# Kernel optimization log

Measured on AMD Instinct MI355X. Metric: run time of the kernel, lower is better.

The kernel has to match this reference:

```python
import jax, jax.numpy as jnp
import numpy as np

NEG_INF = -1e30
D_MODEL = 128


def setup_inputs() -> dict:
    key = jax.random.key(0)
    k1, k2, k3 = jax.random.split(key, 3)
    B, D, Lc, Lq = 64, D_MODEL, 1024, 256
    C = jax.random.normal(k1, (B, D, Lc), dtype=jnp.float32)
    Q = jax.random.normal(k2, (B, D, Lq), dtype=jnp.float32)
    cmask = jnp.ones((B, Lc), dtype=jnp.float32)
    qmask = jnp.ones((B, Lq), dtype=jnp.float32)
    lim = (1.0 / D) ** 0.5
    w = jax.random.uniform(k3, (3 * D,), dtype=jnp.float32, minval=-lim, maxval=lim)
    return {"C": C, "Q": Q, "cmask": cmask, "qmask": qmask, "w": w}


def reference(C, Q, cmask, qmask, w):
    # C: (B, D, Lc), Q: (B, D, Lq), w: (3D,)
    D = C.shape[1]
    Ct = jnp.swapaxes(C, 1, 2)  # (B, Lc, D)
    Qt = jnp.swapaxes(Q, 1, 2)  # (B, Lq, D)
    w1, w2, w3 = w[:D], w[D:2 * D], w[2 * D:]
    # Decomposed trilinear similarity: equivalent to cat([Ct,Qt,Ct*Qt]) @ w
    S = (jnp.einsum('bld,d->bl', Ct, w1)[:, :, None]
         + jnp.einsum('bmd,d->bm', Qt, w2)[:, None, :]
         + jnp.einsum('bld,bmd->blm', Ct * w3, Qt))  # (B, Lc, Lq)
    qm = qmask[:, None, :]  # (B, 1, Lq)
    cm = cmask[:, :, None]  # (B, Lc, 1)
    S1 = jax.nn.softmax(S + (1.0 - qm) * NEG_INF, axis=2)
    S2 = jax.nn.softmax(S + (1.0 - cm) * NEG_INF, axis=1)
    A = jnp.einsum('blm,bmd->bld', S1, Qt)  # (B, Lc, D)
    S12 = jnp.einsum('blm,bnm->bln', S1, S2)  # (B, Lc, Lc)
    Bv = jnp.einsum('bln,bnd->bld', S12, Ct)  # (B, Lc, D)
    out = jnp.concatenate([Ct, A, Ct * A, Ct * Bv], axis=2)  # (B, Lc, 4D)
    # dropout is identity in eval mode
    return jnp.swapaxes(out, 1, 2)  # (B, 4D, Lc)
```

## Files before the change

### kernel.cpp

```cpp
#include <hip/hip_runtime.h>

#define NB  64
#define ND  128
#define NLC 1024
#define NLQ 256
#define FNEG (-1e30f)

typedef __bf16 bf16x8 __attribute__((ext_vector_type(8)));
typedef float f32x4 __attribute__((ext_vector_type(4)));

__device__ __forceinline__ ushort f2bf(float x) {
  unsigned u = __float_as_uint(x);
  return (ushort)((u + 0x7fffu + ((u >> 16) & 1u)) >> 16);
}
__device__ __forceinline__ float bf2f(ushort u) {
  return __uint_as_float((unsigned)u << 16);
}
__device__ __forceinline__ bf16x8 ldfrag(const ushort* p) {
  return *reinterpret_cast<const bf16x8*>(p);
}
__device__ __forceinline__ uint4 pack8(float a0, float a1, float a2, float a3,
                                       float a4, float a5, float a6, float a7) {
  uint4 pk;
  pk.x = (unsigned)f2bf(a0) | ((unsigned)f2bf(a1) << 16);
  pk.y = (unsigned)f2bf(a2) | ((unsigned)f2bf(a3) << 16);
  pk.z = (unsigned)f2bf(a4) | ((unsigned)f2bf(a5) << 16);
  pk.w = (unsigned)f2bf(a6) | ((unsigned)f2bf(a7) << 16);
  return pk;
}

__global__ __launch_bounds__(256) void convert_kernel(
    const float* __restrict__ C, const float* __restrict__ Q,
    const float* __restrict__ w,
    ushort* __restrict__ Ctw3, ushort* __restrict__ Qt16,
    ushort* __restrict__ Cn16, ushort* __restrict__ Qn16,
    float* __restrict__ c1part, float* __restrict__ q2part) {
  __shared__ float tile[64][65];
  __shared__ float cred[64][4];
  int b = blockIdx.y;
  int tid = blockIdx.x;
  int t = threadIdx.x, c = t & 63, r0 = t >> 6;
  if (tid < 32) {
    int d0 = (tid >> 4) * 64, l0 = (tid & 15) * 64;
    const float* src = C + (size_t)b * ND * NLC;
    float part = 0.f;
#pragma unroll
    for (int p = 0; p < 16; ++p) {
      int r = r0 + p * 4;
      float v = src[(size_t)(d0 + r) * NLC + l0 + c];
      tile[c][r] = v * w[2 * ND + d0 + r];
      part += v * w[d0 + r];
    }
    cred[c][r0] = part;
    __syncthreads();
    ushort* dst = Ctw3 + (size_t)b * NLC * ND;
#pragma unroll
    for (int p = 0; p < 16; ++p) {
      int r = r0 + p * 4;
      dst[(size_t)(l0 + r) * ND + d0 + c] = f2bf(tile[r][c]);
    }
    if (t < 64)
      c1part[(size_t)(tid >> 4) * NB * NLC + b * NLC + l0 + t] =
          cred[t][0] + cred[t][1] + cred[t][2] + cred[t][3];
  } else if (tid < 40) {
    int q = tid - 32;
    int d0 = (q >> 2) * 64, m0 = (q & 3) * 64;
    const float* src = Q + (size_t)b * ND * NLQ;
    float part = 0.f;
#pragma unroll
    for (int p = 0; p < 16; ++p) {
      int r = r0 + p * 4;
      float v = src[(size_t)(d0 + r) * NLQ + m0 + c];
      tile[c][r] = v;
      part += v * w[ND + d0 + r];
    }
    cred[c][r0] = part;
    __syncthreads();
    ushort* dst = Qt16 + (size_t)b * NLQ * ND;
#pragma unroll
    for (int p = 0; p < 16; ++p) {
      int r = r0 + p * 4;
      dst[(size_t)(m0 + r) * ND + d0 + c] = f2bf(tile[r][c]);
    }
    if (t < 64)
      q2part[(size_t)(q >> 2) * NB * NLQ + b * NLQ + m0 + t] =
          cred[t][0] + cred[t][1] + cred[t][2] + cred[t][3];
  } else if (tid < 56) {
    size_t ofs = (size_t)(tid - 40) * 8192;
    const float* src = C + (size_t)b * ND * NLC + ofs;
    ushort* dst = Cn16 + (size_t)b * ND * NLC + ofs;
#pragma unroll
    for (int it = 0; it < 4; ++it) {
      int e = (it * 256 + t) * 8;
      float4 v0 = *(const float4*)(src + e), v1 = *(const float4*)(src + e + 4);
      *(uint4*)(dst + e) = pack8(v0.x, v0.y, v0.z, v0.w, v1.x, v1.y, v1.z, v1.w);
    }
  } else {
    size_t ofs = (size_t)(tid - 56) * 16384;
    const float* src = Q + (size_t)b * ND * NLQ + ofs;
    ushort* dst = Qn16 + (size_t)b * ND * NLQ + ofs;
#pragma unroll
    for (int it = 0; it < 8; ++it) {
      int e = (it * 256 + t) * 8;
      float4 v0 = *(const float4*)(src + e), v1 = *(const float4*)(src + e + 4);
      *(uint4*)(dst + e) = pack8(v0.x, v0.y, v0.z, v0.w, v1.x, v1.y, v1.z, v1.w);
    }
  }
}

__global__ __launch_bounds__(512) void score_stats(
    const ushort* __restrict__ Ctw3, const ushort* __restrict__ Qt16,
    const float* __restrict__ c1part, const float* __restrict__ q2part,
    const float* __restrict__ cmask, const float* __restrict__ qmask,
    ushort* __restrict__ e1g, ushort* __restrict__ e1t,
    float* __restrict__ rscale_g, float* __restrict__ psum_part,
    float* __restrict__ chunkmax_g) {
  __shared__ union {
    struct { __align__(16) ushort As[128 * 32]; __align__(16) ushort Bs[256 * 32]; } s;
    __align__(16) ushort bounce[128 * 264];
    __align__(16) ushort bounce2[256 * 136];
  } u;
  __shared__ float rowred[128][4];
  __shared__ float rowsum[128][4];
  __shared__ float colred[256][2];
  __shared__ float rmaxs[128];
  __shared__ float rcs[128];
  __shared__ float cnegs[128];
  __shared__ float qnegs[256];
  __shared__ float c1s[128];
  __shared__ float q2s[256];
  __shared__ float chunkmax_s;

  int b = blockIdx.y, chunk = blockIdx.x, l0 = chunk * 128;
  int t = threadIdx.x, lane = t & 63, wid = t >> 6;
  int wy = wid >> 2, wx = wid & 3, ln = lane & 15, qd = lane >> 4;

  if (t < 128) {
    int idx = b * NLC + l0 + t;
    c1s[t] = c1part[idx] + c1part[NB * NLC + idx];
    cnegs[t] = (1.f - cmask[idx]) * FNEG;
  } else if (t < 384) {
    int m = t - 128;
    int idx = b * NLQ + m;
    q2s[m] = q2part[idx] + q2part[NB * NLQ + idx];
    qnegs[m] = (1.f - qmask[idx]) * FNEG;
  }

  const ushort* Ab = Ctw3 + (size_t)b * NLC * ND;
  const ushort* Bb = Qt16 + (size_t)b * NLQ * ND;
  f32x4 acc[4][4];
#pragma unroll
  for (int i = 0; i < 4; ++i)
#pragma unroll
    for (int j = 0; j < 4; ++j) acc[i][j] = (f32x4){0.f, 0.f, 0.f, 0.f};

  for (int kk = 0; kk < ND; kk += 32) {
#pragma unroll
    for (int p = 0; p < 3; ++p) {
      int e4 = p * 512 + t;
      if (e4 < 512) {
        int r = e4 >> 2, cc = (e4 & 3) * 8;
        *(int4*)(u.s.As + r * 32 + cc) = *(const int4*)(Ab + (size_t)(l0 + r) * ND + kk + cc);
      } else {
        int e = e4 - 512;
        int r = e >> 2, cc = (e & 3) * 8;
        *(int4*)(u.s.Bs + r * 32 + cc) = *(const int4*)(Bb + (size_t)r * ND + kk + cc);
      }
    }
    __syncthreads();
    bf16x8 af[4], bfr[4];
#pragma unroll
    for (int i = 0; i < 4; ++i) {
      af[i]  = ldfrag(u.s.As + (wy * 64 + i * 16 + ln) * 32 + qd * 8);
      bfr[i] = ldfrag(u.s.Bs + (wx * 64 + i * 16 + ln) * 32 + qd * 8);
    }
#pragma unroll
    for (int i = 0; i < 4; ++i)
#pragma unroll
      for (int j = 0; j < 4; ++j)
        acc[i][j] = __builtin_amdgcn_mfma_f32_16x16x32_bf16(af[i], bfr[j], acc[i][j], 0, 0, 0);
    __syncthreads();
  }

  float qnj[4], q2j[4];
#pragma unroll
  for (int j = 0; j < 4; ++j) {
    int m = wx * 64 + j * 16 + ln;
    qnj[j] = qnegs[m];
    q2j[j] = q2s[m];
  }
#pragma unroll
  for (int i = 0; i < 4; ++i)
#pragma unroll
    for (int r = 0; r < 4; ++r) {
      int ll = wy * 64 + i * 16 + qd * 4 + r;
      float cv = c1s[ll];
#pragma unroll
      for (int j = 0; j < 4; ++j) acc[i][j][r] += cv + q2j[j];
    }

#pragma unroll
  for (int i = 0; i < 4; ++i)
#pragma unroll
    for (int r = 0; r < 4; ++r) {
      float v = -INFINITY;
#pragma unroll
      for (int j = 0; j < 4; ++j) v = fmaxf(v, acc[i][j][r] + qnj[j]);
      v = fmaxf(v, __shfl_xor(v, 1));
      v = fmaxf(v, __shfl_xor(v, 2));
      v = fmaxf(v, __shfl_xor(v, 4));
      v = fmaxf(v, __shfl_xor(v, 8));
      if (ln == 0) rowred[wy * 64 + i * 16 + qd * 4 + r][wx] = v;
    }
  __syncthreads();
  if (t < 128) {
    float v = fmaxf(fmaxf(rowred[t][0], rowred[t][1]), fmaxf(rowred[t][2], rowred[t][3]));
    rmaxs[t] = v;
    rcs[t] = v + cnegs[t];
  }
  __syncthreads();
  if (t < 64) {
    float v = fmaxf(rcs[t], rcs[t + 64]);
    v = fmaxf(v, __shfl_xor(v, 1));
    v = fmaxf(v, __shfl_xor(v, 2));
    v = fmaxf(v, __shfl_xor(v, 4));
    v = fmaxf(v, __shfl_xor(v, 8));
    v = fmaxf(v, __shfl_xor(v, 16));
    v = fmaxf(v, __shfl_xor(v, 32));
    if (t == 0) chunkmax_s = v;
  }
  __syncthreads();
  if (t < 128) rcs[t] = __expf(rcs[t] - chunkmax_s);
  __syncthreads();

  float cs[4] = {0.f, 0.f, 0.f, 0.f};
#pragma unroll
  for (int i = 0; i < 4; ++i)
#pragma unroll
    for (int r = 0; r < 4; ++r) {
      int ll = wy * 64 + i * 16 + qd * 4 + r;
      float rmx = rmaxs[ll], rf = rcs[ll];
      float rs = 0.f;
#pragma unroll
      for (int j = 0; j < 4; ++j) {
        float e = __expf(acc[i][j][r] + qnj[j] - rmx);
        acc[i][j][r] = e;
        rs += e;
        cs[j] += e * rf;
      }
      rs += __shfl_xor(rs, 1);
      rs += __shfl_xor(rs, 2);
      rs += __shfl_xor(rs, 4);
      rs += __shfl_xor(rs, 8);
      if (ln == 0) rowsum[ll][wx] = rs;
    }
#pragma unroll
  for (int j = 0; j < 4; ++j) {
    float v = cs[j];
    v += __shfl_xor(v, 16);
    v += __shfl_xor(v, 32);
    if (qd == 0) colred[wx * 64 + j * 16 + ln][wy] = v;
  }
  __syncthreads();
  if (t < 128)
    rscale_g[b * NLC + l0 + t] =
        1.f / (rowsum[t][0] + rowsum[t][1] + rowsum[t][2] + rowsum[t][3]);
  if (t >= 256 && t < 512) {
    int m = t - 256;
    psum_part[(b * 8 + chunk) * NLQ + m] = colred[m][0] + colred[m][1];
  }
  if (t == 0) chunkmax_g[b * 8 + chunk] = chunkmax_s;

#pragma unroll
  for (int i = 0; i < 4; ++i)
#pragma unroll
    for (int r = 0; r < 4; ++r) {
      int ll = wy * 64 + i * 16 + qd * 4 + r;
#pragma unroll
      for (int j = 0; j < 4; ++j)
        u.bounce[ll * 264 + wx * 64 + j * 16 + ln] = f2bf(acc[i][j][r]);
    }
  __syncthreads();
  ushort* Eb = e1g + (size_t)b * NLC * NLQ;
#pragma unroll
  for (int p = 0; p < 8; ++p) {
    int idx4 = p * 512 + t;
    int r = idx4 >> 5, c = (idx4 & 31) * 8;
    *(int4*)(Eb + (size_t)(l0 + r) * NLQ + c) = *(const int4*)(u.bounce + r * 264 + c);
  }
  __syncthreads();

#pragma unroll
  for (int i = 0; i < 4; ++i)
#pragma unroll
    for (int r = 0; r < 4; ++r) {
      int ll = wy * 64 + i * 16 + qd * 4 + r;
      float rf = rcs[ll];
#pragma unroll
      for (int j = 0; j < 4; ++j)
        u.bounce2[(wx * 64 + j * 16 + ln) * 136 + ll] = f2bf(acc[i][j][r] * rf);
    }
  __syncthreads();
  ushort* Etb = e1t + (size_t)b * NLQ * NLC;
#pragma unroll
  for (int p = 0; p < 8; ++p) {
    int idx4 = p * 512 + t;
    int m = idx4 >> 4, l8 = idx4 & 15;
    *(int4*)(Etb + (size_t)m * NLC + l0 + l8 * 8) =
        *(const int4*)(u.bounce2 + m * 136 + l8 * 8);
  }
}

__global__ __launch_bounds__(256) void stat_combine(
    const float* __restrict__ psum_part, const float* __restrict__ chunkmax_g,
    float* __restrict__ cinv) {
  __shared__ float cm[8];
  int b = blockIdx.x, t = threadIdx.x;
  if (t < 8) cm[t] = chunkmax_g[b * 8 + t];
  __syncthreads();
  float K = cm[0];
#pragma unroll
  for (int c = 1; c < 8; ++c) K = fmaxf(K, cm[c]);
  float s = 0.f;
#pragma unroll
  for (int c = 0; c < 8; ++c)
    s += psum_part[(b * 8 + c) * NLQ + t] * __expf(cm[c] - K);
  cinv[b * NLQ + t] = 1.f / s;
}

__global__ __launch_bounds__(512) void tmat_mfma(
    const ushort* __restrict__ Cn16, const ushort* __restrict__ e1t,
    const float* __restrict__ chunkmax_g, float* __restrict__ Tpart) {
  __shared__ __align__(16) ushort As[128 * 32];
  __shared__ __align__(16) ushort Bs[256 * 32];
  int b = blockIdx.y, ks = blockIdx.x;
  int t = threadIdx.x, lane = t & 63, wid = t >> 6;
  int wy = wid >> 2, wx = wid & 3, ln = lane & 15, qd = lane >> 4;
  const ushort* Cb = Cn16 + (size_t)b * ND * NLC;
  const ushort* Eb = e1t + (size_t)b * NLQ * NLC;
  float cm0 = chunkmax_g[b * 8 + 2 * ks];
  float cm1 = chunkmax_g[b * 8 + 2 * ks + 1];
  int first = (cm0 <= cm1) ? 0 : 1;
  float resc = __expf(fminf(cm0, cm1) - fmaxf(cm0, cm1));
  f32x4 acc[4][4];
#pragma unroll
  for (int i = 0; i < 4; ++i)
#pragma unroll
    for (int j = 0; j < 4; ++j) acc[i][j] = (f32x4){0.f, 0.f, 0.f, 0.f};

  for (int h = 0; h < 2; ++h) {
    int lbase = (2 * ks + (h ? 1 - first : first)) * 128;
    for (int c0 = 0; c0 < 128; c0 += 32) {
#pragma unroll
      for (int p = 0; p < 3; ++p) {
        int e4 = p * 512 + t;
        if (e4 < 512) {
          int r = e4 >> 2, cc = (e4 & 3) * 8;
          *(int4*)(As + r * 32 + cc) =
              *(const int4*)(Cb + (size_t)r * NLC + lbase + c0 + cc);
        } else {
          int e = e4 - 512;
          int rm = e >> 2, cc = (e & 3) * 8;
          *(int4*)(Bs + rm * 32 + cc) =
              *(const int4*)(Eb + (size_t)rm * NLC + lbase + c0 + cc);
        }
      }
      __syncthreads();
      bf16x8 af[4], bfr[4];
#pragma unroll
      for (int i = 0; i < 4; ++i) {
        af[i]  = ldfrag(As + (wy * 64 + i * 16 + ln) * 32 + qd * 8);
        bfr[i] = ldfrag(Bs + (wx * 64 + i * 16 + ln) * 32 + qd * 8);
      }
#pragma unroll
      for (int i = 0; i < 4; ++i)
#pragma unroll
        for (int j = 0; j < 4; ++j)
          acc[i][j] = __builtin_amdgcn_mfma_f32_16x16x32_bf16(af[i], bfr[j], acc[i][j], 0, 0, 0);
      __syncthreads();
    }
    if (h == 0) {
#pragma unroll
      for (int i = 0; i < 4; ++i)
#pragma unroll
        for (int j = 0; j < 4; ++j)
#pragma unroll
          for (int r = 0; r < 4; ++r) acc[i][j][r] *= resc;
    }
  }
  float* Tb = Tpart + ((size_t)(b * 4 + ks)) * ND * NLQ;
#pragma unroll
  for (int i = 0; i < 4; ++i)
#pragma unroll
    for (int r = 0; r < 4; ++r) {
      int d = wy * 64 + i * 16 + qd * 4 + r;
#pragma unroll
      for (int j = 0; j < 4; ++j) {
        int m = wx * 64 + j * 16 + ln;
        Tb[(size_t)d * NLQ + m] = acc[i][j][r];
      }
    }
}

__global__ __launch_bounds__(256) void tcombine(
    const float* __restrict__ Tpart, const float* __restrict__ cinv,
    const float* __restrict__ chunkmax_g, ushort* __restrict__ Tt) {
  int gid = blockIdx.x * 256 + threadIdx.x;
  int e = gid * 4;
  int b = e >> 15;
  int r = e & 32767;
  int m = r & 255;
  const float* cmb = chunkmax_g + b * 8;
  float K = cmb[0];
#pragma unroll
  for (int c = 1; c < 8; ++c) K = fmaxf(K, cmb[c]);
  float4 s = {0.f, 0.f, 0.f, 0.f};
#pragma unroll
  for (int ks = 0; ks < 4; ++ks) {
    float fac = __expf(fmaxf(cmb[2 * ks], cmb[2 * ks + 1]) - K);
    float4 v = *(const float4*)(Tpart + ((size_t)(b * 4 + ks)) * ND * NLQ + r);
    s.x += fac * v.x; s.y += fac * v.y; s.z += fac * v.z; s.w += fac * v.w;
  }
  float4 ci = *(const float4*)(cinv + b * NLQ + m);
  ushort4 o;
  o.x = f2bf(s.x * ci.x); o.y = f2bf(s.y * ci.y);
  o.z = f2bf(s.z * ci.z); o.w = f2bf(s.w * ci.w);
  *(ushort4*)(Tt + (size_t)b * ND * NLQ + r) = o;
}

__global__ __launch_bounds__(256, 2) void outk(
    const float* __restrict__ C, const ushort* __restrict__ Qn16,
    const ushort* __restrict__ Tt, const ushort* __restrict__ e1g,
    const float* __restrict__ rscale, float* __restrict__ out) {
  __shared__ __align__(16) ushort As1[128 * 32];
  __shared__ __align__(16) ushort As2[128 * 32];
  __shared__ __align__(16) ushort Bs[128 * 32];
  int b = blockIdx.y;
  int l0 = blockIdx.x * 128;
  const ushort* Qb = Qn16 + (size_t)b * ND * NLQ;
  const ushort* Tb = Tt + (size_t)b * ND * NLQ;
  const ushort* Eb = e1g + (size_t)b * NLC * NLQ;
  int t = threadIdx.x, lane = t & 63, wid = t >> 6, wy = wid >> 1, wx = wid & 1;
  int ln = lane & 15, qd = lane >> 4;
  f32x4 acc1[4][4], acc2[4][4];
#pragma unroll
  for (int i = 0; i < 4; ++i)
#pragma unroll
    for (int j = 0; j < 4; ++j) {
      acc1[i][j] = (f32x4){0.f, 0.f, 0.f, 0.f};
      acc2[i][j] = (f32x4){0.f, 0.f, 0.f, 0.f};
    }

  for (int m0 = 0; m0 < NLQ; m0 += 32) {
#pragma unroll
    for (int p = 0; p < 2; ++p) {
      int e = t * 8 + p * 2048;
      int r = e >> 5, cc = e & 31;
      *(int4*)(As1 + e) = *(const int4*)(Qb + (size_t)r * NLQ + m0 + cc);
      *(int4*)(As2 + e) = *(const int4*)(Tb + (size_t)r * NLQ + m0 + cc);
      *(int4*)(Bs + e)  = *(const int4*)(Eb + (size_t)(l0 + r) * NLQ + m0 + cc);
    }
    __syncthreads();
    bf16x8 a1[4], a2[4], bfr[4];
#pragma unroll
    for (int i = 0; i < 4; ++i) {
      a1[i] = ldfrag(As1 + (wy * 64 + i * 16 + ln) * 32 + qd * 8);
      a2[i] = ldfrag(As2 + (wy * 64 + i * 16 + ln) * 32 + qd * 8);
      bfr[i] = ldfrag(Bs + (wx * 64 + i * 16 + ln) * 32 + qd * 8);
    }
#pragma unroll
    for (int i = 0; i < 4; ++i)
#pragma unroll
      for (int j = 0; j < 4; ++j) {
        acc1[i][j] = __builtin_amdgcn_mfma_f32_16x16x32_bf16(a1[i], bfr[j], acc1[i][j], 0, 0, 0);
        acc2[i][j] = __builtin_amdgcn_mfma_f32_16x16x32_bf16(a2[i], bfr[j], acc2[i][j], 0, 0, 0);
      }
    __syncthreads();
  }

  const float* Cb = C + (size_t)b * ND * NLC;
  float* outb = out + (size_t)b * 4 * ND * NLC;
#pragma unroll
  for (int j = 0; j < 4; ++j) {
    int l = l0 + wx * 64 + j * 16 + ln;
    float rs = rscale[b * NLC + l];
#pragma unroll
    for (int i = 0; i < 4; ++i)
#pragma unroll
      for (int r = 0; r < 4; ++r) {
        int d = wy * 64 + i * 16 + qd * 4 + r;
        float a = acc1[i][j][r] * rs;
        float bv = acc2[i][j][r] * rs;
        float c = Cb[(size_t)d * NLC + l];
        outb[(size_t)d * NLC + l] = c;
        outb[(size_t)(128 + d) * NLC + l] = a;
        outb[(size_t)(256 + d) * NLC + l] = c * a;
        outb[(size_t)(384 + d) * NLC + l] = c * bv;
      }
  }
}

extern "C" void kernel_launch(void* const* d_in, const int* in_sizes, int n_in,
                              void* d_out, int out_size, void* d_ws, size_t ws_size,
                              hipStream_t stream) {
  const float* C     = (const float*)d_in[0];
  const float* Q     = (const float*)d_in[1];
  const float* cmask = (const float*)d_in[2];
  const float* qmask = (const float*)d_in[3];
  const float* w     = (const float*)d_in[4];
  float* out = (float*)d_out;

  char* p = (char*)d_ws;
  auto alloc = [&](size_t bytes) { char* r = p; p += (bytes + 255) & ~(size_t)255; return r; };
  ushort* e1g    = (ushort*)alloc((size_t)NB * NLC * NLQ * 2);
  ushort* e1t    = (ushort*)alloc((size_t)NB * NLQ * NLC * 2);
  ushort* Ctw3   = (ushort*)alloc((size_t)NB * NLC * ND * 2);
  ushort* Qt16   = (ushort*)alloc((size_t)NB * NLQ * ND * 2);
  ushort* Cn16   = (ushort*)alloc((size_t)NB * ND * NLC * 2);
  ushort* Qn16   = (ushort*)alloc((size_t)NB * ND * NLQ * 2);
  float*  Tpart  = (float*)alloc((size_t)NB * 4 * ND * NLQ * 4);
  ushort* Tt     = (ushort*)alloc((size_t)NB * ND * NLQ * 2);
  float*  c1part = (float*)alloc((size_t)2 * NB * NLC * 4);
  float*  q2part = (float*)alloc((size_t)2 * NB * NLQ * 4);
  float*  rscale = (float*)alloc((size_t)NB * NLC * 4);
  float*  cinv   = (float*)alloc((size_t)NB * NLQ * 4);
  float*  psum   = (float*)alloc((size_t)NB * 8 * NLQ * 4);
  float*  chmax  = (float*)alloc((size_t)NB * 8 * 4);

  convert_kernel<<<dim3(58, NB), 256, 0, stream>>>(C, Q, w, Ctw3, Qt16, Cn16, Qn16,
                                                   c1part, q2part);
  score_stats<<<dim3(NLC / 128, NB), 512, 0, stream>>>(
      Ctw3, Qt16, c1part, q2part, cmask, qmask, e1g, e1t, rscale, psum, chmax);
  stat_combine<<<NB, 256, 0, stream>>>(psum, chmax, cinv);
  tmat_mfma<<<dim3(4, NB), 512, 0, stream>>>(Cn16, e1t, chmax, Tpart);
  tcombine<<<(NB * ND * NLQ / 4) / 256, 256, 0, stream>>>(Tpart, cinv, chmax, Tt);
  outk<<<dim3(NLC / 128, NB), 256, 0, stream>>>(C, Qn16, Tt, e1g, rscale, out);
}
```

Before: 307.0 us.

## Fuse T-matrix GEMM into score kernel and widen output kernel tiles

The score kernel now multiplies each chunk's scaled exp tile (already in shared memory) by the matching slab of C, writing per-chunk partial T products. This removes the transposed e1t global buffer, its write and re-read, and the separate tmat_mfma launch. tcombine now reduces 8 chunk partials instead of 4, which doubles the Tpart traffic. The output kernel also moves to 512-thread blocks covering 256 context positions, which halves the repeated loads of the Q and T tiles.

```diff
diff --git a/kernel.cpp b/kernel.cpp
--- a/kernel.cpp
+++ b/kernel.cpp
@@ -110,15 +110,16 @@
 
 __global__ __launch_bounds__(512) void score_stats(
     const ushort* __restrict__ Ctw3, const ushort* __restrict__ Qt16,
+    const ushort* __restrict__ Cn16,
     const float* __restrict__ c1part, const float* __restrict__ q2part,
     const float* __restrict__ cmask, const float* __restrict__ qmask,
-    ushort* __restrict__ e1g, ushort* __restrict__ e1t,
-    float* __restrict__ rscale_g, float* __restrict__ psum_part,
-    float* __restrict__ chunkmax_g) {
+    ushort* __restrict__ e1g, float* __restrict__ rscale_g,
+    float* __restrict__ psum_part, float* __restrict__ chunkmax_g,
+    float* __restrict__ Tpart) {
   __shared__ union {
     struct { __align__(16) ushort As[128 * 32]; __align__(16) ushort Bs[256 * 32]; } s;
     __align__(16) ushort bounce[128 * 264];
-    __align__(16) ushort bounce2[256 * 136];
+    struct { __align__(16) ushort bounce2[256 * 136]; __align__(16) ushort As_c[4 * 128 * 32]; } t2;
   } u;
   __shared__ float rowred[128][4];
   __shared__ float rowsum[128][4];
@@ -298,17 +299,51 @@
       float rf = rcs[ll];
 #pragma unroll
       for (int j = 0; j < 4; ++j)
-        u.bounce2[(wx * 64 + j * 16 + ln) * 136 + ll] = f2bf(acc[i][j][r] * rf);
-    }
-  __syncthreads();
-  ushort* Etb = e1t + (size_t)b * NLQ * NLC;
-#pragma unroll
-  for (int p = 0; p < 8; ++p) {
-    int idx4 = p * 512 + t;
-    int m = idx4 >> 4, l8 = idx4 & 15;
-    *(int4*)(Etb + (size_t)m * NLC + l0 + l8 * 8) =
-        *(const int4*)(u.bounce2 + m * 136 + l8 * 8);
-  }
+        u.t2.bounce2[(wx * 64 + j * 16 + ln) * 136 + ll] = f2bf(acc[i][j][r] * rf);
+    }
+  {
+    const ushort* Cb = Cn16 + (size_t)b * ND * NLC;
+#pragma unroll
+    for (int p = 0; p < 4; ++p) {
+      int e4 = p * 512 + t;
+      int slab = e4 >> 9, rr = (e4 >> 2) & 127, cc = (e4 & 3) * 8;
+      *(int4*)(u.t2.As_c + slab * (128 * 32) + rr * 32 + cc) =
+          *(const int4*)(Cb + (size_t)rr * NLC + l0 + slab * 32 + cc);
+    }
+  }
+  __syncthreads();
+  f32x4 acc2[4][4];
+#pragma unroll
+  for (int i = 0; i < 4; ++i)
+#pragma unroll
+    for (int j = 0; j < 4; ++j) acc2[i][j] = (f32x4){0.f, 0.f, 0.f, 0.f};
+#pragma unroll
+  for (int kk = 0; kk < 4; ++kk) {
+    bf16x8 af2[4], bf2[4];
+#pragma unroll
+    for (int i = 0; i < 4; ++i)
+      af2[i] = ldfrag(u.t2.As_c + kk * (128 * 32) + (wy * 64 + i * 16 + ln) * 32 + qd * 8);
+#pragma unroll
+    for (int j = 0; j < 4; ++j)
+      bf2[j] = ldfrag(u.t2.bounce2 + (wx * 64 + j * 16 + ln) * 136 + kk * 32 + qd * 8);
+#pragma unroll
+    for (int i = 0; i < 4; ++i)
+#pragma unroll
+      for (int j = 0; j < 4; ++j)
+        acc2[i][j] = __builtin_amdgcn_mfma_f32_16x16x32_bf16(af2[i], bf2[j], acc2[i][j], 0, 0, 0);
+  }
+  float* Tb = Tpart + (size_t)(b * 8 + chunk) * ND * NLQ;
+#pragma unroll
+  for (int i = 0; i < 4; ++i)
+#pragma unroll
+    for (int r = 0; r < 4; ++r) {
+      int d = wy * 64 + i * 16 + qd * 4 + r;
+#pragma unroll
+      for (int j = 0; j < 4; ++j) {
+        int m = wx * 64 + j * 16 + ln;
+        Tb[(size_t)d * NLQ + m] = acc2[i][j][r];
+      }
+    }
 }
 
 __global__ __launch_bounds__(256) void stat_combine(
@@ -326,80 +361,6 @@
   for (int c = 0; c < 8; ++c)
     s += psum_part[(b * 8 + c) * NLQ + t] * __expf(cm[c] - K);
   cinv[b * NLQ + t] = 1.f / s;
-}
-
-__global__ __launch_bounds__(512) void tmat_mfma(
-    const ushort* __restrict__ Cn16, const ushort* __restrict__ e1t,
-    const float* __restrict__ chunkmax_g, float* __restrict__ Tpart) {
-  __shared__ __align__(16) ushort As[128 * 32];
-  __shared__ __align__(16) ushort Bs[256 * 32];
-  int b = blockIdx.y, ks = blockIdx.x;
-  int t = threadIdx.x, lane = t & 63, wid = t >> 6;
-  int wy = wid >> 2, wx = wid & 3, ln = lane & 15, qd = lane >> 4;
-  const ushort* Cb = Cn16 + (size_t)b * ND * NLC;
-  const ushort* Eb = e1t + (size_t)b * NLQ * NLC;
-  float cm0 = chunkmax_g[b * 8 + 2 * ks];
-  float cm1 = chunkmax_g[b * 8 + 2 * ks + 1];
-  int first = (cm0 <= cm1) ? 0 : 1;
-  float resc = __expf(fminf(cm0, cm1) - fmaxf(cm0, cm1));
-  f32x4 acc[4][4];
-#pragma unroll
-  for (int i = 0; i < 4; ++i)
-#pragma unroll
-    for (int j = 0; j < 4; ++j) acc[i][j] = (f32x4){0.f, 0.f, 0.f, 0.f};
-
-  for (int h = 0; h < 2; ++h) {
-    int lbase = (2 * ks + (h ? 1 - first : first)) * 128;
-    for (int c0 = 0; c0 < 128; c0 += 32) {
-#pragma unroll
-      for (int p = 0; p < 3; ++p) {
-        int e4 = p * 512 + t;
-        if (e4 < 512) {
-          int r = e4 >> 2, cc = (e4 & 3) * 8;
-          *(int4*)(As + r * 32 + cc) =
-              *(const int4*)(Cb + (size_t)r * NLC + lbase + c0 + cc);
-        } else {
-          int e = e4 - 512;
-          int rm = e >> 2, cc = (e & 3) * 8;
-          *(int4*)(Bs + rm * 32 + cc) =
-              *(const int4*)(Eb + (size_t)rm * NLC + lbase + c0 + cc);
-        }
-      }
-      __syncthreads();
-      bf16x8 af[4], bfr[4];
-#pragma unroll
-      for (int i = 0; i < 4; ++i) {
-        af[i]  = ldfrag(As + (wy * 64 + i * 16 + ln) * 32 + qd * 8);
-        bfr[i] = ldfrag(Bs + (wx * 64 + i * 16 + ln) * 32 + qd * 8);
-      }
-#pragma unroll
-      for (int i = 0; i < 4; ++i)
-#pragma unroll
-        for (int j = 0; j < 4; ++j)
-          acc[i][j] = __builtin_amdgcn_mfma_f32_16x16x32_bf16(af[i], bfr[j], acc[i][j], 0, 0, 0);
-      __syncthreads();
-    }
-    if (h == 0) {
-#pragma unroll
-      for (int i = 0; i < 4; ++i)
-#pragma unroll
-        for (int j = 0; j < 4; ++j)
-#pragma unroll
-          for (int r = 0; r < 4; ++r) acc[i][j][r] *= resc;
-    }
-  }
-  float* Tb = Tpart + ((size_t)(b * 4 + ks)) * ND * NLQ;
-#pragma unroll
-  for (int i = 0; i < 4; ++i)
-#pragma unroll
-    for (int r = 0; r < 4; ++r) {
-      int d = wy * 64 + i * 16 + qd * 4 + r;
-#pragma unroll
-      for (int j = 0; j < 4; ++j) {
-        int m = wx * 64 + j * 16 + ln;
-        Tb[(size_t)d * NLQ + m] = acc[i][j][r];
-      }
-    }
 }
 
 __global__ __launch_bounds__(256) void tcombine(
@@ -416,9 +377,9 @@
   for (int c = 1; c < 8; ++c) K = fmaxf(K, cmb[c]);
   float4 s = {0.f, 0.f, 0.f, 0.f};
 #pragma unroll
-  for (int ks = 0; ks < 4; ++ks) {
-    float fac = __expf(fmaxf(cmb[2 * ks], cmb[2 * ks + 1]) - K);
-    float4 v = *(const float4*)(Tpart + ((size_t)(b * 4 + ks)) * ND * NLQ + r);
+  for (int c = 0; c < 8; ++c) {
+    float fac = __expf(cmb[c] - K);
+    float4 v = *(const float4*)(Tpart + ((size_t)(b * 8 + c)) * ND * NLQ + r);
     s.x += fac * v.x; s.y += fac * v.y; s.z += fac * v.z; s.w += fac * v.w;
   }
   float4 ci = *(const float4*)(cinv + b * NLQ + m);
@@ -428,19 +389,19 @@
   *(ushort4*)(Tt + (size_t)b * ND * NLQ + r) = o;
 }
 
-__global__ __launch_bounds__(256, 2) void outk(
+__global__ __launch_bounds__(512) void outk(
     const float* __restrict__ C, const ushort* __restrict__ Qn16,
     const ushort* __restrict__ Tt, const ushort* __restrict__ e1g,
     const float* __restrict__ rscale, float* __restrict__ out) {
   __shared__ __align__(16) ushort As1[128 * 32];
   __shared__ __align__(16) ushort As2[128 * 32];
-  __shared__ __align__(16) ushort Bs[128 * 32];
+  __shared__ __align__(16) ushort Bs[256 * 32];
   int b = blockIdx.y;
-  int l0 = blockIdx.x * 128;
+  int l0 = blockIdx.x * 256;
   const ushort* Qb = Qn16 + (size_t)b * ND * NLQ;
   const ushort* Tb = Tt + (size_t)b * ND * NLQ;
   const ushort* Eb = e1g + (size_t)b * NLC * NLQ;
-  int t = threadIdx.x, lane = t & 63, wid = t >> 6, wy = wid >> 1, wx = wid & 1;
+  int t = threadIdx.x, lane = t & 63, wid = t >> 6, wy = wid >> 2, wx = wid & 3;
   int ln = lane & 15, qd = lane >> 4;
   f32x4 acc1[4][4], acc2[4][4];
 #pragma unroll
@@ -452,13 +413,16 @@
     }
 
   for (int m0 = 0; m0 < NLQ; m0 += 32) {
+    {
+      int r = t >> 2, cc = (t & 3) * 8;
+      *(int4*)(As1 + r * 32 + cc) = *(const int4*)(Qb + (size_t)r * NLQ + m0 + cc);
+      *(int4*)(As2 + r * 32 + cc) = *(const int4*)(Tb + (size_t)r * NLQ + m0 + cc);
+    }
 #pragma unroll
     for (int p = 0; p < 2; ++p) {
-      int e = t * 8 + p * 2048;
-      int r = e >> 5, cc = e & 31;
-      *(int4*)(As1 + e) = *(const int4*)(Qb + (size_t)r * NLQ + m0 + cc);
-      *(int4*)(As2 + e) = *(const int4*)(Tb + (size_t)r * NLQ + m0 + cc);
-      *(int4*)(Bs + e)  = *(const int4*)(Eb + (size_t)(l0 + r) * NLQ + m0 + cc);
+      int e4 = p * 512 + t;
+      int r = e4 >> 2, cc = (e4 & 3) * 8;
+      *(int4*)(Bs + r * 32 + cc) = *(const int4*)(Eb + (size_t)(l0 + r) * NLQ + m0 + cc);
     }
     __syncthreads();
     bf16x8 a1[4], a2[4], bfr[4];
@@ -513,12 +477,11 @@
   char* p = (char*)d_ws;
   auto alloc = [&](size_t bytes) { char* r = p; p += (bytes + 255) & ~(size_t)255; return r; };
   ushort* e1g    = (ushort*)alloc((size_t)NB * NLC * NLQ * 2);
-  ushort* e1t    = (ushort*)alloc((size_t)NB * NLQ * NLC * 2);
   ushort* Ctw3   = (ushort*)alloc((size_t)NB * NLC * ND * 2);
   ushort* Qt16   = (ushort*)alloc((size_t)NB * NLQ * ND * 2);
   ushort* Cn16   = (ushort*)alloc((size_t)NB * ND * NLC * 2);
   ushort* Qn16   = (ushort*)alloc((size_t)NB * ND * NLQ * 2);
-  float*  Tpart  = (float*)alloc((size_t)NB * 4 * ND * NLQ * 4);
+  float*  Tpart  = (float*)alloc((size_t)NB * 8 * ND * NLQ * 4);
   ushort* Tt     = (ushort*)alloc((size_t)NB * ND * NLQ * 2);
   float*  c1part = (float*)alloc((size_t)2 * NB * NLC * 4);
   float*  q2part = (float*)alloc((size_t)2 * NB * NLQ * 4);
@@ -530,9 +493,8 @@
   convert_kernel<<<dim3(58, NB), 256, 0, stream>>>(C, Q, w, Ctw3, Qt16, Cn16, Qn16,
                                                    c1part, q2part);
   score_stats<<<dim3(NLC / 128, NB), 512, 0, stream>>>(
-      Ctw3, Qt16, c1part, q2part, cmask, qmask, e1g, e1t, rscale, psum, chmax);
+      Ctw3, Qt16, Cn16, c1part, q2part, cmask, qmask, e1g, rscale, psum, chmax, Tpart);
   stat_combine<<<NB, 256, 0, stream>>>(psum, chmax, cinv);
-  tmat_mfma<<<dim3(4, NB), 512, 0, stream>>>(Cn16, e1t, chmax, Tpart);
   tcombine<<<(NB * ND * NLQ / 4) / 256, 256, 0, stream>>>(Tpart, cinv, chmax, Tt);
-  outk<<<dim3(NLC / 128, NB), 256, 0, stream>>>(C, Qn16, Tt, e1g, rscale, out);
-}
+  outk<<<dim3(NLC / 256, NB), 512, 0, stream>>>(C, Qn16, Tt, e1g, rscale, out);
+}
```

Result: no change. 307.0 us (-0.0%).
